# Kernel tuning notes

Measured on AMD Instinct MI355X. Metric: run time of the kernel, lower is better.

Reference implementation:

```python
import jax, jax.numpy as jnp
import numpy as np

CHUNK = 128      # chunk_size
SAMPLE = 16      # sample_size -> at most SAMPLE chunks selected per row


def sinusoidal_pe(T, H):
    # standard transformer sinusoidal positional encoding [T, H]
    pos = jnp.arange(T, dtype=jnp.float32)[:, None]
    div = jnp.exp(jnp.arange(0, H, 2, dtype=jnp.float32) * (-np.log(10000.0) / H))
    pe = jnp.zeros((T, H), dtype=jnp.float32)
    pe = pe.at[:, 0::2].set(jnp.sin(pos * div))
    pe = pe.at[:, 1::2].set(jnp.cos(pos * div))
    return pe


def setup_inputs() -> dict:
    key = jax.random.key(0)
    k1, k2, k3, k4 = jax.random.split(key, 4)
    B, T, D, H = 8, 8192, 1024, 1024
    data = jax.random.normal(k1, (B, T, D), jnp.float32)
    state = jax.random.normal(k2, (B, 64, H), jnp.float32)
    W = jax.random.normal(k3, (D, H), jnp.float32) / np.sqrt(D)
    b = jnp.zeros((H,), jnp.float32)
    chunk_idx = jax.random.randint(k4, (B, SAMPLE), 0, T // CHUNK)  # sampled chunks
    return {"state": state, "data": data, "W": W, "b": b, "chunk_idx": chunk_idx}


def reference(state, data, W, b, chunk_idx):
    B, T, D = data.shape
    H = W.shape[1]
    n_chunks = T // CHUNK
    # add_pos: linear embed + positional encoding, scaled by sqrt(chunk_size)
    x = (data @ W + b + sinusoidal_pe(T, H)[None]) * np.sqrt(CHUNK)  # [B,T,H]
    # union of SAMPLE one-hot chunk selections (== StochasticMultinomialTensor sample .max(1))
    onehot = jax.nn.one_hot(chunk_idx, n_chunks, dtype=jnp.float32)   # [B,SAMPLE,n_chunks]
    mask_c = onehot.max(axis=1)                                       # [B,n_chunks] in {0,1}
    mask = jnp.repeat(mask_c, CHUNK, axis=1)                          # [B,T]
    lens = mask.sum(axis=1).astype(jnp.int32)                         # selected token counts
    # stable left-alignment: selected positions first, original order preserved
    order = jnp.argsort(1.0 - mask, axis=1, stable=True)              # [B,T]
    Smax = SAMPLE * CHUNK                                             # static max length
    order = order[:, :Smax]
    gathered = jnp.take_along_axis(x, order[..., None], axis=1)       # [B,Smax,H]
    valid = (jnp.arange(Smax)[None, :] < lens[:, None]).astype(x.dtype)
    # selected tokens scaled by F value (=1.0); padding zeroed (pad_sequence semantics)
    return gathered * valid[..., None]
```

## Files before the change

### kernel.cpp

```cpp
#include <hip/hip_runtime.h>
#include <hip/hip_fp16.h>
#include <math.h>

#define NB 8
#define NT 8192
#define ND 1024
#define NH 1024
#define CHUNK_ 128
#define SAMPLE_ 16
#define NCHUNK 64
#define SMAX 2048
#define MROWS (NB * SMAX)
#define BK 64

typedef _Float16 half8 __attribute__((ext_vector_type(8)));
typedef float floatx4 __attribute__((ext_vector_type(4)));
typedef unsigned short ushort8 __attribute__((ext_vector_type(8)));

__device__ __attribute__((aligned(16))) unsigned short g_Wt[(size_t)NH * ND];
__device__ __attribute__((aligned(16))) unsigned short g_A[(size_t)MROWS * ND];

__device__ __forceinline__ unsigned short f2h(float f) {
  return __half_as_ushort(__float2half(f));
}

__device__ __forceinline__ int slot_t0(const int* __restrict__ cidx, int b, int slot) {
  unsigned long long m = 0ull;
#pragma unroll
  for (int j = 0; j < SAMPLE_; ++j) m |= (1ull << (cidx[b * SAMPLE_ + j] & 63));
  unsigned long long tmp = m;
  for (int s = 0; s < slot; ++s) tmp &= (tmp - 1ull);
  if (tmp == 0ull) return -1;
  return (__ffsll((unsigned long long)tmp) - 1) * CHUNK_;
}

__global__ __launch_bounds__(256) void k_prep(const float* __restrict__ W,
                                              const float* __restrict__ data,
                                              const int* __restrict__ cidx) {
  if (blockIdx.x < 256) {
    __shared__ unsigned short tile[64][65];
    const int hb = (blockIdx.x & 15) * 64;
    const int db = (blockIdx.x >> 4) * 64;
    const int c = threadIdx.x & 63;
    const int r0 = threadIdx.x >> 6;
#pragma unroll
    for (int j = 0; j < 16; ++j) {
      const int r = r0 + j * 4;
      tile[c][r] = f2h(W[(size_t)(db + r) * NH + hb + c]);
    }
    __syncthreads();
#pragma unroll
    for (int j = 0; j < 16; ++j) {
      const int r = r0 + j * 4;
      g_Wt[(size_t)(hb + r) * ND + db + c] = tile[r][c];
    }
    return;
  }

  const int row0 = (blockIdx.x - 256) * 2;
  const int b = row0 >> 11;
  const int slot = (row0 >> 7) & 15;
  const int t0 = slot_t0(cidx, b, slot);
  if (t0 < 0) return;

  const int sub = threadIdx.x >> 7;
  const int row = row0 + sub;
  const int t = t0 + (row0 & 127) + sub;
  const int col = (threadIdx.x & 127) * 8;
  const float4* src = (const float4*)(data + ((size_t)b * NT + t) * ND + col);
  const float4 v0 = src[0];
  const float4 v1 = src[1];
  ushort8 o;
  o[0] = f2h(v0.x); o[1] = f2h(v0.y); o[2] = f2h(v0.z); o[3] = f2h(v0.w);
  o[4] = f2h(v1.x); o[5] = f2h(v1.y); o[6] = f2h(v1.z); o[7] = f2h(v1.w);
  *(ushort8*)(g_A + (size_t)row * ND + col) = o;
}

__device__ __forceinline__ void gl_lds16(const unsigned short* g, unsigned short* l) {
  __builtin_amdgcn_global_load_lds(
      (const __attribute__((address_space(1))) unsigned int*)g,
      (__attribute__((address_space(3))) unsigned int*)l, 16, 0, 0);
}

__global__ __launch_bounds__(256) void k_gemm(const float* __restrict__ bias,
                                              const int* __restrict__ cidx,
                                              float* __restrict__ out) {
  __shared__ unsigned short As[128 * BK];
  __shared__ unsigned short Bs[128 * BK];

  const int tid = threadIdx.x;
  const int tile_n = blockIdx.x & 7;
  const int tile_m = blockIdx.x >> 3;
  const int t0 = slot_t0(cidx, tile_m >> 4, tile_m & 15);

  if (t0 < 0) {
    const int r = tid >> 1;
    const int cb = (tid & 1) * 64;
    float4 z = make_float4(0.f, 0.f, 0.f, 0.f);
    float* o = out + (size_t)(tile_m * 128 + r) * NH + tile_n * 128 + cb;
#pragma unroll
    for (int v = 0; v < 16; ++v) *(float4*)(o + 4 * v) = z;
    return;
  }

  const int lane = tid & 63;
  const int w = tid >> 6;
  const int wm = w & 1;
  const int wn = w >> 1;

  floatx4 acc[4][4];
#pragma unroll
  for (int i = 0; i < 4; ++i)
#pragma unroll
    for (int j = 0; j < 4; ++j) acc[i][j] = (floatx4){0.f, 0.f, 0.f, 0.f};

  const int srow = lane >> 3;
  const int g8 = (((lane & 7) ^ srow) * 8);
  const unsigned short* gA0 =
      g_A + (size_t)(tile_m * 128 + w * 32 + srow) * ND + g8;
  const unsigned short* gB0 =
      g_Wt + (size_t)(tile_n * 128 + w * 32 + srow) * ND + g8;
  unsigned short* lA0 = As + w * 2048;
  unsigned short* lB0 = Bs + w * 2048;

  const int mrow = wm * 64 + (lane & 15);
  const int nrow = wn * 64 + (lane & 15);
  const int x7 = lane & 7;
  int aoff[4][2], boff[4][2];
#pragma unroll
  for (int i = 0; i < 4; ++i)
#pragma unroll
    for (int s = 0; s < 2; ++s) {
      const int c = ((lane >> 4) + s * 4) ^ x7;
      aoff[i][s] = (mrow + i * 16) * BK + c * 8;
      boff[i][s] = (nrow + i * 16) * BK + c * 8;
    }

  for (int kk = 0; kk < ND; kk += BK) {
    __syncthreads();
#pragma unroll
    for (int q = 0; q < 4; ++q) gl_lds16(gA0 + (size_t)q * 8 * ND + kk, lA0 + q * 512);
#pragma unroll
    for (int q = 0; q < 4; ++q) gl_lds16(gB0 + (size_t)q * 8 * ND + kk, lB0 + q * 512);
    __syncthreads();

#pragma unroll
    for (int s = 0; s < 2; ++s) {
      half8 af[4], bf[4];
#pragma unroll
      for (int i = 0; i < 4; ++i) af[i] = *(const half8*)(As + aoff[i][s]);
#pragma unroll
      for (int j = 0; j < 4; ++j) bf[j] = *(const half8*)(Bs + boff[j][s]);
#pragma unroll
      for (int i = 0; i < 4; ++i)
#pragma unroll
        for (int j = 0; j < 4; ++j)
          acc[i][j] = __builtin_amdgcn_mfma_f32_16x16x32_f16(af[i], bf[j], acc[i][j], 0, 0, 0);
    }
  }

  const float scale = 11.313708498984761f;
  const float nl = -9.210340371976184f / 1024.f;
  const int colq = lane & 15;
  const int rq = (lane >> 4) * 4;
#pragma unroll
  for (int j = 0; j < 4; ++j) {
    const int gh = tile_n * 128 + wn * 64 + j * 16 + colq;
    const float freq = __expf((float)(gh & ~1) * nl);
    const float bv = bias[gh];
#pragma unroll
    for (int i = 0; i < 4; ++i) {
      const int lrow0 = wm * 64 + i * 16 + rq;
#pragma unroll
      for (int r = 0; r < 4; ++r) {
        const int lrow = lrow0 + r;
        const float arg = (float)(t0 + lrow) * freq;
        const float pe = (gh & 1) ? __cosf(arg) : __sinf(arg);
        out[(size_t)(tile_m * 128 + lrow) * NH + gh] =
            (acc[i][j][r] + bv + pe) * scale;
      }
    }
  }
}

extern "C" void kernel_launch(void* const* d_in, const int* in_sizes, int n_in,
                              void* d_out, int out_size, void* d_ws, size_t ws_size,
                              hipStream_t stream) {
  (void)d_ws; (void)ws_size;
  const float* data = (const float*)d_in[1];
  const float* W = (const float*)d_in[2];
  const float* bias = (const float*)d_in[3];
  const int* cidx = (const int*)d_in[4];
  float* out = (float*)d_out;

  k_prep<<<256 + MROWS / 2, 256, 0, stream>>>(W, data, cidx);
  k_gemm<<<(MROWS / 128) * (NH / 128), 256, 0, stream>>>(bias, cidx, out);
}
```

Before: 387.5 us.

## Restructure GEMM into 256x256 tiles with 8 waves and software-pipelined LDS staging

The GEMM kernel moves from 128x128 tiles with 4 waves to 256x256 tiles with 8 waves. It splits each K step into four quarter phases that interleave global-to-LDS prefetch of the next K tile with MFMA on the current one, using fine-grained waitcnt/barrier control and s_setprio. Dynamic LDS (80KB) double-buffers the B operand. This targets the load-compute serialization and lower data reuse of the old single-buffered loop. In exchange it uses more registers, gives coarser handling of empty slots, and leaves fewer blocks to fill the GPU.

Result: faster. 379.8 us (-2.0%).

```diff
diff --git a/kernel.cpp b/kernel.cpp
--- a/kernel.cpp
+++ b/kernel.cpp
@@ -8,7 +8,6 @@
 #define NH 1024
 #define CHUNK_ 128
 #define SAMPLE_ 16
-#define NCHUNK 64
 #define SMAX 2048
 #define MROWS (NB * SMAX)
 #define BK 64
@@ -82,24 +81,26 @@
       (__attribute__((address_space(3))) unsigned int*)l, 16, 0, 0);
 }
 
-__global__ __launch_bounds__(256) void k_gemm(const float* __restrict__ bias,
-                                              const int* __restrict__ cidx,
-                                              float* __restrict__ out) {
-  __shared__ unsigned short As[128 * BK];
-  __shared__ unsigned short Bs[128 * BK];
+__global__ __launch_bounds__(512, 2) void k_gemm(const float* __restrict__ bias,
+                                                 const int* __restrict__ cidx,
+                                                 float* __restrict__ out) {
+  extern __shared__ unsigned short lds[];
 
   const int tid = threadIdx.x;
-  const int tile_n = blockIdx.x & 7;
-  const int tile_m = blockIdx.x >> 3;
-  const int t0 = slot_t0(cidx, tile_m >> 4, tile_m & 15);
-
-  if (t0 < 0) {
-    const int r = tid >> 1;
-    const int cb = (tid & 1) * 64;
+  const int tile_n = blockIdx.x & 3;
+  const int tile_m = blockIdx.x >> 2;
+  const int slot_even = tile_m * 2;
+  const int b0 = slot_even >> 4;
+  const int t0e = slot_t0(cidx, b0, slot_even & 15);
+
+  if (t0e < 0) {
     float4 z = make_float4(0.f, 0.f, 0.f, 0.f);
-    float* o = out + (size_t)(tile_m * 128 + r) * NH + tile_n * 128 + cb;
-#pragma unroll
-    for (int v = 0; v < 16; ++v) *(float4*)(o + 4 * v) = z;
+    float* obase = out + (size_t)tile_m * 256 * NH + tile_n * 256;
+#pragma unroll
+    for (int v = 0; v < 32; ++v) {
+      const int f = v * 512 + tid;
+      *(float4*)(obase + (size_t)(f >> 6) * NH + (f & 63) * 4) = z;
+    }
     return;
   }
 
@@ -107,78 +108,174 @@
   const int w = tid >> 6;
   const int wm = w & 1;
   const int wn = w >> 1;
-
-  floatx4 acc[4][4];
-#pragma unroll
-  for (int i = 0; i < 4; ++i)
+  const int t0w = wm ? slot_t0(cidx, b0, (slot_even + 1) & 15) : t0e;
+
+  floatx4 acc[8][4];
+#pragma unroll
+  for (int i = 0; i < 8; ++i)
 #pragma unroll
     for (int j = 0; j < 4; ++j) acc[i][j] = (floatx4){0.f, 0.f, 0.f, 0.f};
 
   const int srow = lane >> 3;
-  const int g8 = (((lane & 7) ^ srow) * 8);
-  const unsigned short* gA0 =
-      g_A + (size_t)(tile_m * 128 + w * 32 + srow) * ND + g8;
-  const unsigned short* gB0 =
-      g_Wt + (size_t)(tile_n * 128 + w * 32 + srow) * ND + g8;
-  unsigned short* lA0 = As + w * 2048;
-  unsigned short* lB0 = Bs + w * 2048;
-
-  const int mrow = wm * 64 + (lane & 15);
-  const int nrow = wn * 64 + (lane & 15);
+  const int v8 = w * 8 + srow;
+  const int u8 = (v8 & 31) + (v8 >> 5) * 64;
+  const int gch = ((lane & 7) ^ srow) * 8;
+  const unsigned short* gA = g_A + (size_t)(tile_m * 256) * ND + gch;
+  const unsigned short* gB = g_Wt + (size_t)(tile_n * 256) * ND + gch;
+  unsigned short* dA = lds + w * 512;
+  unsigned short* dB = lds + 16384 + w * 512;
+
+#define STAGE_AX(KT)                                                       \
+  do {                                                                     \
+    const unsigned short* s_ = gA + (size_t)v8 * ND + (KT)*BK;             \
+    gl_lds16(s_, dA);                                                      \
+    gl_lds16(s_ + (size_t)128 * ND, dA + 4096);                            \
+  } while (0)
+#define STAGE_AY(KT)                                                       \
+  do {                                                                     \
+    const unsigned short* s_ = gA + (size_t)(v8 + 64) * ND + (KT)*BK;      \
+    gl_lds16(s_, dA + 8192);                                               \
+    gl_lds16(s_ + (size_t)128 * ND, dA + 8192 + 4096);                     \
+  } while (0)
+#define STAGE_BX(P, KT)                                                    \
+  do {                                                                     \
+    const unsigned short* s_ = gB + (size_t)u8 * ND + (KT)*BK;             \
+    unsigned short* d_ = dB + (P)*8192;                                    \
+    gl_lds16(s_, d_);                                                      \
+    gl_lds16(s_ + (size_t)128 * ND, d_ + 4096);                            \
+  } while (0)
+#define STAGE_BY(KT)                                                       \
+  do {                                                                     \
+    const unsigned short* s_ = gB + (size_t)(u8 + 32) * ND + (KT)*BK;      \
+    gl_lds16(s_, dB + 16384);                                              \
+    gl_lds16(s_ + (size_t)128 * ND, dB + 16384 + 4096);                    \
+  } while (0)
+
+  const int fr = lane & 15;
   const int x7 = lane & 7;
-  int aoff[4][2], boff[4][2];
-#pragma unroll
-  for (int i = 0; i < 4; ++i)
-#pragma unroll
-    for (int s = 0; s < 2; ++s) {
-      const int c = ((lane >> 4) + s * 4) ^ x7;
-      aoff[i][s] = (mrow + i * 16) * BK + c * 8;
-      boff[i][s] = (nrow + i * 16) * BK + c * 8;
-    }
-
-  for (int kk = 0; kk < ND; kk += BK) {
-    __syncthreads();
-#pragma unroll
-    for (int q = 0; q < 4; ++q) gl_lds16(gA0 + (size_t)q * 8 * ND + kk, lA0 + q * 512);
-#pragma unroll
-    for (int q = 0; q < 4; ++q) gl_lds16(gB0 + (size_t)q * 8 * ND + kk, lB0 + q * 512);
-    __syncthreads();
-
-#pragma unroll
-    for (int s = 0; s < 2; ++s) {
-      half8 af[4], bf[4];
-#pragma unroll
-      for (int i = 0; i < 4; ++i) af[i] = *(const half8*)(As + aoff[i][s]);
-#pragma unroll
-      for (int j = 0; j < 4; ++j) bf[j] = *(const half8*)(Bs + boff[j][s]);
-#pragma unroll
-      for (int i = 0; i < 4; ++i)
-#pragma unroll
-        for (int j = 0; j < 4; ++j)
-          acc[i][j] = __builtin_amdgcn_mfma_f32_16x16x32_f16(af[i], bf[j], acc[i][j], 0, 0, 0);
-    }
-  }
-
-  const float scale = 11.313708498984761f;
-  const float nl = -9.210340371976184f / 1024.f;
-  const int colq = lane & 15;
-  const int rq = (lane >> 4) * 4;
-#pragma unroll
-  for (int j = 0; j < 4; ++j) {
-    const int gh = tile_n * 128 + wn * 64 + j * 16 + colq;
-    const float freq = __expf((float)(gh & ~1) * nl);
-    const float bv = bias[gh];
-#pragma unroll
-    for (int i = 0; i < 4; ++i) {
-      const int lrow0 = wm * 64 + i * 16 + rq;
-#pragma unroll
-      for (int r = 0; r < 4; ++r) {
-        const int lrow = lrow0 + r;
-        const float arg = (float)(t0 + lrow) * freq;
-        const float pe = (gh & 1) ? __cosf(arg) : __sinf(arg);
-        out[(size_t)(tile_m * 128 + lrow) * NH + gh] =
-            (acc[i][j][r] + bv + pe) * scale;
+  int aoff[8][2], boff[4][2];
+#pragma unroll
+  for (int s = 0; s < 2; ++s) {
+    const int ck = ((((lane >> 4) + s * 4)) ^ x7) * 8;
+#pragma unroll
+    for (int i = 0; i < 8; ++i)
+      aoff[i][s] = (i >> 2) * 8192 + ((i & 3) * 16 + fr + wm * 64) * 64 + ck;
+#pragma unroll
+    for (int j = 0; j < 4; ++j)
+      boff[j][s] = ((j >> 1) ? 32768 : 16384) + ((j & 1) * 16 + fr + wn * 32) * 64 + ck;
+  }
+
+  half8 a[4][2], b[2][2];
+
+#define LOADA(MH)                                                          \
+  do {                                                                     \
+    _Pragma("unroll") for (int i4 = 0; i4 < 4; ++i4)                       \
+    _Pragma("unroll") for (int s = 0; s < 2; ++s)                          \
+        a[i4][s] = *(const half8*)(lds + aoff[(MH)*4 + i4][s]);            \
+  } while (0)
+#define LOADB0(BXO)                                                        \
+  do {                                                                     \
+    _Pragma("unroll") for (int j2 = 0; j2 < 2; ++j2)                       \
+    _Pragma("unroll") for (int s = 0; s < 2; ++s)                          \
+        b[j2][s] = *(const half8*)(lds + boff[j2][s] + (BXO));             \
+  } while (0)
+#define LOADB1()                                                           \
+  do {                                                                     \
+    _Pragma("unroll") for (int j2 = 0; j2 < 2; ++j2)                       \
+    _Pragma("unroll") for (int s = 0; s < 2; ++s)                          \
+        b[j2][s] = *(const half8*)(lds + boff[2 + j2][s]);                 \
+  } while (0)
+#define MFMAQ(MH, NQ)                                                      \
+  do {                                                                     \
+    __builtin_amdgcn_s_setprio(1);                                         \
+    _Pragma("unroll") for (int s = 0; s < 2; ++s)                          \
+    _Pragma("unroll") for (int i4 = 0; i4 < 4; ++i4)                       \
+    _Pragma("unroll") for (int j2 = 0; j2 < 2; ++j2)                       \
+        acc[(MH)*4 + i4][(NQ)*2 + j2] =                                    \
+            __builtin_amdgcn_mfma_f32_16x16x32_f16(                        \
+                a[i4][s], b[j2][s], acc[(MH)*4 + i4][(NQ)*2 + j2], 0, 0, 0); \
+    __builtin_amdgcn_s_setprio(0);                                         \
+  } while (0)
+#define MIDSYNC()                                                          \
+  do {                                                                     \
+    __builtin_amdgcn_sched_barrier(0);                                     \
+    __builtin_amdgcn_s_barrier();                                          \
+    asm volatile("s_waitcnt lgkmcnt(0)" ::: "memory");                     \
+    __builtin_amdgcn_sched_barrier(0);                                     \
+  } while (0)
+#define ENDSYNC()                                                          \
+  do {                                                                     \
+    __builtin_amdgcn_sched_barrier(0);                                     \
+    asm volatile("s_waitcnt vmcnt(4)" ::: "memory");                       \
+    __builtin_amdgcn_s_barrier();                                          \
+    __builtin_amdgcn_sched_barrier(0);                                     \
+  } while (0)
+
+  STAGE_BX(0, 0);
+  STAGE_AX(0);
+  STAGE_BY(0);
+  STAGE_AY(0);
+  __builtin_amdgcn_sched_barrier(0);
+  asm volatile("s_waitcnt vmcnt(4)" ::: "memory");
+  __builtin_amdgcn_s_barrier();
+  __builtin_amdgcn_sched_barrier(0);
+
+  for (int t = 0; t < 16; ++t) {
+    const int bx = (t & 1) * 8192;
+    const int pn = (t + 1) & 1;
+    const int tn = (t < 15) ? t + 1 : 15;
+    LOADA(0);
+    LOADB0(bx);
+    STAGE_BX(pn, tn);
+    MIDSYNC();
+    MFMAQ(0, 0);
+    ENDSYNC();
+    LOADB1();
+    STAGE_AX(tn);
+    MIDSYNC();
+    MFMAQ(0, 1);
+    ENDSYNC();
+    LOADA(1);
+    STAGE_BY(tn);
+    MIDSYNC();
+    MFMAQ(1, 1);
+    ENDSYNC();
+    LOADB0(bx);
+    STAGE_AY(tn);
+    MIDSYNC();
+    MFMAQ(1, 0);
+    ENDSYNC();
+  }
+
+  if (t0w >= 0) {
+    const float scale = 11.313708498984761f;
+    const float nl = -9.210340371976184f / 1024.f;
+    const int colq = lane & 15;
+    const int rq = (lane >> 4) * 4;
+#pragma unroll
+    for (int j = 0; j < 4; ++j) {
+      const int gh = tile_n * 256 + wn * 64 + j * 16 + colq;
+      const float freq = __expf((float)(gh & ~1) * nl);
+      const float bv = bias[gh];
+#pragma unroll
+      for (int i = 0; i < 8; ++i) {
+#pragma unroll
+        for (int r = 0; r < 4; ++r) {
+          const int lrow = i * 16 + rq + r;
+          const float arg = (float)(t0w + lrow) * freq;
+          const float pe = (gh & 1) ? __cosf(arg) : __sinf(arg);
+          out[(size_t)(tile_m * 256 + wm * 128 + lrow) * NH + gh] =
+              (acc[i][j][r] + bv + pe) * scale;
+        }
       }
+    }
+  } else {
+    float4 z = make_float4(0.f, 0.f, 0.f, 0.f);
+    float* obase = out + (size_t)(tile_m * 256 + wm * 128) * NH + tile_n * 256 + wn * 64;
+#pragma unroll
+    for (int v = 0; v < 32; ++v) {
+      const int f = v * 64 + lane;
+      *(float4*)(obase + (size_t)(f >> 4) * NH + (f & 15) * 4) = z;
     }
   }
 }
@@ -187,6 +284,12 @@
                               void* d_out, int out_size, void* d_ws, size_t ws_size,
                               hipStream_t stream) {
   (void)d_ws; (void)ws_size;
+  static bool s_init = false;
+  if (!s_init) {
+    hipFuncSetAttribute(reinterpret_cast<const void*>(k_gemm),
+                        hipFuncAttributeMaxDynamicSharedMemorySize, 81920);
+    s_init = true;
+  }
   const float* data = (const float*)d_in[1];
   const float* W = (const float*)d_in[2];
   const float* bias = (const float*)d_in[3];
@@ -194,5 +297,5 @@
   float* out = (float*)d_out;
 
   k_prep<<<256 + MROWS / 2, 256, 0, stream>>>(W, data, cidx);
-  k_gemm<<<(MROWS / 128) * (NH / 128), 256, 0, stream>>>(bias, cidx, out);
-}
+  k_gemm<<<(MROWS / 256) * (NH / 256), 512, 81920, stream>>>(bias, cidx, out);
+}
```
